# Performance work log

Hardware: AMD Instinct MI355X
Metric: run time of the kernel (lower is better)

## Reference

```python
import jax, jax.numpy as jnp
import numpy as np

UP_TIME = 1440.0
UP_DIST = 40.0
LOC_CNT = 100000
LOC_LEN = 131072
H = 256


def setup_inputs() -> dict:
    key = jax.random.key(0)
    ks = jax.random.split(key, 12)
    stdv = 1.0 / np.sqrt(H)
    u = lambda k, shape: jax.random.uniform(k, shape, jnp.float32, -stdv, stdv)
    return {
        "td_upper": jax.random.uniform(ks[0], (LOC_LEN,), jnp.float32),
        "td_lower": jax.random.uniform(ks[1], (LOC_LEN,), jnp.float32),
        "ld_upper": jax.random.uniform(ks[2], (LOC_LEN,), jnp.float32),
        "ld_lower": jax.random.uniform(ks[3], (LOC_LEN,), jnp.float32),
        "loc": jax.random.randint(ks[4], (LOC_LEN,), 0, LOC_CNT, jnp.int32),
        "hx": jax.random.normal(ks[5], (H, 1), jnp.float32),
        "weight_ih": u(ks[6], (H, H)),
        "weight_th_upper": u(ks[7], (H, H)),
        "weight_th_lower": u(ks[8], (H, H)),
        "weight_sh_upper": u(ks[9], (H, H)),
        "weight_sh_lower": u(ks[10], (H, H)),
        "location_weight": u(ks[11], (LOC_CNT, H)),
    }


def reference(td_upper, td_lower, ld_upper, ld_lower, loc, hx,
              weight_ih, weight_th_upper, weight_th_lower,
              weight_sh_upper, weight_sh_lower, location_weight):
    tu = jnp.clip(td_upper, 0.0, UP_TIME)
    tl = jnp.clip(td_lower, 0.0, UP_TIME)
    lu = jnp.clip(ld_upper, 0.0, UP_DIST)
    ll = jnp.clip(ld_lower, 0.0, UP_DIST)

    e = location_weight[loc]  # [L, H] gathered POI embeddings
    # Ttd[i] @ e[i] = (tu[i]*W_tu@e[i] + tl[i]*W_tl@e[i]) / (tu[i]+tl[i])
    a = jnp.einsum('hk,lk->lh', weight_th_upper, e)
    b = jnp.einsum('hk,lk->lh', weight_th_lower, e)
    t = (tu[:, None] * a + tl[:, None] * b) / (tu + tl)[:, None]  # [L, H]
    # Sld[i] @ t[i]
    c = jnp.einsum('hk,lk->lh', weight_sh_upper, t)
    d = jnp.einsum('hk,lk->lh', weight_sh_lower, t)
    s = (lu[:, None] * c + ll[:, None] * d) / (lu + ll)[:, None]  # [L, H]

    loc_vec = jnp.sum(s, axis=0)[:, None]  # [H, 1]
    usr_vec = weight_ih @ hx               # [H, 1]
    return jax.nn.sigmoid(loc_vec + usr_vec)
```

## Files before the change

kernel.cpp:

```cpp
#include <hip/hip_runtime.h>
#include <math.h>

#define H 256

__global__ __launch_bounds__(256) void strnn_scatter(
    const float* __restrict__ td_u, const float* __restrict__ td_l,
    const float* __restrict__ ld_u, const float* __restrict__ ld_l,
    const int* __restrict__ loc, float* __restrict__ W, int L, int Rpad)
{
    const int i = blockIdx.x * blockDim.x + threadIdx.x;
    if (i >= L) return;
    const float tu = fminf(fmaxf(td_u[i], 0.f), 1440.f);
    const float tl = fminf(fmaxf(td_l[i], 0.f), 1440.f);
    const float lu = fminf(fmaxf(ld_u[i], 0.f), 40.f);
    const float ll = fminf(fmaxf(ld_l[i], 0.f), 40.f);
    const float al = tu / (tu + tl);
    const float be = lu / (lu + ll);
    const int r = loc[i];
    atomicAdd(W + r,            be * al);
    atomicAdd(W + Rpad + r,     be * (1.f - al));
    atomicAdd(W + 2 * Rpad + r, (1.f - be) * al);
    atomicAdd(W + 3 * Rpad + r, (1.f - be) * (1.f - al));
}

__global__ __launch_bounds__(512) void strnn_accum(
    const float* __restrict__ W, const float* __restrict__ table,
    float* __restrict__ v, int R, int Rpad)
{
    __shared__ float s_red[8][4][H];
    const int t    = threadIdx.x;
    const int wave = t >> 6;
    const int lane = t & 63;
    const float* __restrict__ W0 = W;
    const float* __restrict__ W1 = W + Rpad;
    const float* __restrict__ W2 = W + 2 * (size_t)Rpad;
    const float* __restrict__ W3 = W + 3 * (size_t)Rpad;

    float4 a0 = {0,0,0,0}, a1 = {0,0,0,0}, a2 = {0,0,0,0}, a3 = {0,0,0,0};

    const int gw     = blockIdx.x * 8 + wave;
    const int stride = gridDim.x * 8 * 8;

    for (int r0 = gw * 8; r0 < R; r0 += stride) {
        float w0[8], w1[8], w2[8], w3[8];
        *(float4*)&w0[0] = *(const float4*)(W0 + r0);
        *(float4*)&w0[4] = *(const float4*)(W0 + r0 + 4);
        *(float4*)&w1[0] = *(const float4*)(W1 + r0);
        *(float4*)&w1[4] = *(const float4*)(W1 + r0 + 4);
        *(float4*)&w2[0] = *(const float4*)(W2 + r0);
        *(float4*)&w2[4] = *(const float4*)(W2 + r0 + 4);
        *(float4*)&w3[0] = *(const float4*)(W3 + r0);
        *(float4*)&w3[4] = *(const float4*)(W3 + r0 + 4);

        float4 e[8];
        #pragma unroll
        for (int u = 0; u < 8; ++u) {
            const int r = r0 + u;
            const bool live = (r < R) &&
                (w0[u] != 0.f || w1[u] != 0.f || w2[u] != 0.f || w3[u] != 0.f);
            const size_t roff = live ? (size_t)r * H : (size_t)0;
            e[u] = *(const float4*)(table + roff + 4 * lane);
        }
        #pragma unroll
        for (int u = 0; u < 8; ++u) {
            a0.x = fmaf(w0[u], e[u].x, a0.x);
            a0.y = fmaf(w0[u], e[u].y, a0.y);
            a0.z = fmaf(w0[u], e[u].z, a0.z);
            a0.w = fmaf(w0[u], e[u].w, a0.w);
            a1.x = fmaf(w1[u], e[u].x, a1.x);
            a1.y = fmaf(w1[u], e[u].y, a1.y);
            a1.z = fmaf(w1[u], e[u].z, a1.z);
            a1.w = fmaf(w1[u], e[u].w, a1.w);
            a2.x = fmaf(w2[u], e[u].x, a2.x);
            a2.y = fmaf(w2[u], e[u].y, a2.y);
            a2.z = fmaf(w2[u], e[u].z, a2.z);
            a2.w = fmaf(w2[u], e[u].w, a2.w);
            a3.x = fmaf(w3[u], e[u].x, a3.x);
            a3.y = fmaf(w3[u], e[u].y, a3.y);
            a3.z = fmaf(w3[u], e[u].z, a3.z);
            a3.w = fmaf(w3[u], e[u].w, a3.w);
        }
    }

    *(float4*)&s_red[wave][0][4 * lane] = a0;
    *(float4*)&s_red[wave][1][4 * lane] = a1;
    *(float4*)&s_red[wave][2][4 * lane] = a2;
    *(float4*)&s_red[wave][3][4 * lane] = a3;
    __syncthreads();
    const int col = t & 255;
    #pragma unroll
    for (int cc = 0; cc < 2; ++cc) {
        const int c = (t >> 8) * 2 + cc;
        float s = 0.f;
        #pragma unroll
        for (int w_ = 0; w_ < 8; ++w_)
            s += s_red[w_][c][col];
        atomicAdd(&v[c * H + col], s);
    }
}

__global__ __launch_bounds__(256) void strnn_mid(
    const float* __restrict__ Wtu, const float* __restrict__ Wtl,
    const float* __restrict__ Wih, const float* __restrict__ hx,
    const float* __restrict__ v, float* __restrict__ pqu)
{
    const int wave = (blockIdx.x * blockDim.x + threadIdx.x) >> 6;
    const int lane = threadIdx.x & 63;
    const float* v1 = v;
    const float* v2 = v + H;
    const float* v3 = v + 2 * H;
    const float* v4 = v + 3 * H;

    float p = 0.f, q = 0.f, u = 0.f;
    #pragma unroll
    for (int i = 0; i < H; i += 64) {
        const int k = i + lane;
        const float wtu = Wtu[wave * H + k];
        const float wtl = Wtl[wave * H + k];
        p = fmaf(wtu, v1[k], fmaf(wtl, v2[k], p));
        q = fmaf(wtu, v3[k], fmaf(wtl, v4[k], q));
        u = fmaf(Wih[wave * H + k], hx[k], u);
    }
    #pragma unroll
    for (int off = 32; off > 0; off >>= 1) {
        p += __shfl_down(p, off, 64);
        q += __shfl_down(q, off, 64);
        u += __shfl_down(u, off, 64);
    }
    if (lane == 0) {
        pqu[wave]         = p;
        pqu[H + wave]     = q;
        pqu[2 * H + wave] = u;
    }
}

__global__ __launch_bounds__(256) void strnn_out(
    const float* __restrict__ Wsu, const float* __restrict__ Wsl,
    const float* __restrict__ pqu, float* __restrict__ out)
{
    const int wave = (blockIdx.x * blockDim.x + threadIdx.x) >> 6;
    const int lane = threadIdx.x & 63;
    const float* p = pqu;
    const float* q = pqu + H;
    const float* u = pqu + 2 * H;

    float s = 0.f;
    #pragma unroll
    for (int i = 0; i < H; i += 64) {
        const int k = i + lane;
        s = fmaf(Wsu[wave * H + k], p[k], fmaf(Wsl[wave * H + k], q[k], s));
    }
    #pragma unroll
    for (int off = 32; off > 0; off >>= 1)
        s += __shfl_down(s, off, 64);
    if (lane == 0)
        out[wave] = 1.f / (1.f + expf(-(s + u[wave])));
}

extern "C" void kernel_launch(void* const* d_in, const int* in_sizes, int n_in,
                              void* d_out, int out_size, void* d_ws, size_t ws_size,
                              hipStream_t stream) {
    const float* td_u  = (const float*)d_in[0];
    const float* td_l  = (const float*)d_in[1];
    const float* ld_u  = (const float*)d_in[2];
    const float* ld_l  = (const float*)d_in[3];
    const int*   loc   = (const int*)d_in[4];
    const float* hx    = (const float*)d_in[5];
    const float* Wih   = (const float*)d_in[6];
    const float* Wtu   = (const float*)d_in[7];
    const float* Wtl   = (const float*)d_in[8];
    const float* Wsu   = (const float*)d_in[9];
    const float* Wsl   = (const float*)d_in[10];
    const float* table = (const float*)d_in[11];
    const int L = in_sizes[0];
    const int R = in_sizes[11] / H;
    const int Rpad = (R + 7) & ~7;

    float* W   = (float*)d_ws;
    float* v   = W + 4 * (size_t)Rpad;
    float* pqu = v + 4 * H;

    hipMemsetAsync(W, 0, (4 * (size_t)Rpad + 4 * H) * sizeof(float), stream);

    strnn_scatter<<<(L + 255) / 256, 256, 0, stream>>>(
        td_u, td_l, ld_u, ld_l, loc, W, L, Rpad);
    strnn_accum<<<256, 512, 0, stream>>>(W, table, v, R, Rpad);
    strnn_mid<<<64, 256, 0, stream>>>(Wtu, Wtl, Wih, hx, v, pqu);
    strnn_out<<<64, 256, 0, stream>>>(Wsu, Wsl, pqu, (float*)d_out);
}
```

Before: 203.5 us.

## Pack quantized fixed-point weights into two 64-bit atomics per element

Replaces the four float atomics per sequence element with two 64-bit integer atomics holding 24-bit fixed-point sums of alpha, beta, alpha*beta and a count. The four bilinear weights are rebuilt from those sums in the accumulation kernel. The change also drops the zero-row skip, so every table row is read, and doubles the accum grid with an occupancy hint. It cuts atomic traffic and makes the sums deterministic, but it adds quantization error and removes the branch that avoided loading unused rows.

After: 197.4 us. 3.0% less time.

```diff
diff --git a/kernel.cpp b/kernel.cpp
--- a/kernel.cpp
+++ b/kernel.cpp
@@ -2,11 +2,13 @@
 #include <math.h>
 
 #define H 256
+typedef unsigned long long u64;
 
 __global__ __launch_bounds__(256) void strnn_scatter(
     const float* __restrict__ td_u, const float* __restrict__ td_l,
     const float* __restrict__ ld_u, const float* __restrict__ ld_l,
-    const int* __restrict__ loc, float* __restrict__ W, int L, int Rpad)
+    const int* __restrict__ loc, u64* __restrict__ U1, u64* __restrict__ U2,
+    int L)
 {
     const int i = blockIdx.x * blockDim.x + threadIdx.x;
     if (i >= L) return;
@@ -16,25 +18,22 @@
     const float ll = fminf(fmaxf(ld_l[i], 0.f), 40.f);
     const float al = tu / (tu + tl);
     const float be = lu / (lu + ll);
+    const u64 alq = (u64)(unsigned)(al * 16777216.f + 0.5f);
+    const u64 beq = (u64)(unsigned)(be * 16777216.f + 0.5f);
+    const u64 abq = (u64)(unsigned)(al * be * 16777216.f + 0.5f);
     const int r = loc[i];
-    atomicAdd(W + r,            be * al);
-    atomicAdd(W + Rpad + r,     be * (1.f - al));
-    atomicAdd(W + 2 * Rpad + r, (1.f - be) * al);
-    atomicAdd(W + 3 * Rpad + r, (1.f - be) * (1.f - al));
+    atomicAdd(U1 + r, (alq << 32) | beq);
+    atomicAdd(U2 + r, (abq << 32) | 1ull);
 }
 
-__global__ __launch_bounds__(512) void strnn_accum(
-    const float* __restrict__ W, const float* __restrict__ table,
-    float* __restrict__ v, int R, int Rpad)
+__global__ __launch_bounds__(512, 4) void strnn_accum(
+    const u64* __restrict__ U1, const u64* __restrict__ U2,
+    const float* __restrict__ table, float* __restrict__ v, int R)
 {
     __shared__ float s_red[8][4][H];
     const int t    = threadIdx.x;
     const int wave = t >> 6;
     const int lane = t & 63;
-    const float* __restrict__ W0 = W;
-    const float* __restrict__ W1 = W + Rpad;
-    const float* __restrict__ W2 = W + 2 * (size_t)Rpad;
-    const float* __restrict__ W3 = W + 3 * (size_t)Rpad;
 
     float4 a0 = {0,0,0,0}, a1 = {0,0,0,0}, a2 = {0,0,0,0}, a3 = {0,0,0,0};
 
@@ -42,43 +41,48 @@
     const int stride = gridDim.x * 8 * 8;
 
     for (int r0 = gw * 8; r0 < R; r0 += stride) {
-        float w0[8], w1[8], w2[8], w3[8];
-        *(float4*)&w0[0] = *(const float4*)(W0 + r0);
-        *(float4*)&w0[4] = *(const float4*)(W0 + r0 + 4);
-        *(float4*)&w1[0] = *(const float4*)(W1 + r0);
-        *(float4*)&w1[4] = *(const float4*)(W1 + r0 + 4);
-        *(float4*)&w2[0] = *(const float4*)(W2 + r0);
-        *(float4*)&w2[4] = *(const float4*)(W2 + r0 + 4);
-        *(float4*)&w3[0] = *(const float4*)(W3 + r0);
-        *(float4*)&w3[4] = *(const float4*)(W3 + r0 + 4);
-
+        uint4 q1[4], q2[4];
+        #pragma unroll
+        for (int k = 0; k < 4; ++k) {
+            q1[k] = *(const uint4*)(U1 + r0 + 2 * k);
+            q2[k] = *(const uint4*)(U2 + r0 + 2 * k);
+        }
         float4 e[8];
         #pragma unroll
         for (int u = 0; u < 8; ++u) {
-            const int r = r0 + u;
-            const bool live = (r < R) &&
-                (w0[u] != 0.f || w1[u] != 0.f || w2[u] != 0.f || w3[u] != 0.f);
-            const size_t roff = live ? (size_t)r * H : (size_t)0;
-            e[u] = *(const float4*)(table + roff + 4 * lane);
+            int r = r0 + u;
+            r = (r < R) ? r : (R - 1);
+            e[u] = *(const float4*)(table + (size_t)r * H + 4 * lane);
         }
+        const float S = 5.9604644775390625e-8f;
         #pragma unroll
         for (int u = 0; u < 8; ++u) {
-            a0.x = fmaf(w0[u], e[u].x, a0.x);
-            a0.y = fmaf(w0[u], e[u].y, a0.y);
-            a0.z = fmaf(w0[u], e[u].z, a0.z);
-            a0.w = fmaf(w0[u], e[u].w, a0.w);
-            a1.x = fmaf(w1[u], e[u].x, a1.x);
-            a1.y = fmaf(w1[u], e[u].y, a1.y);
-            a1.z = fmaf(w1[u], e[u].z, a1.z);
-            a1.w = fmaf(w1[u], e[u].w, a1.w);
-            a2.x = fmaf(w2[u], e[u].x, a2.x);
-            a2.y = fmaf(w2[u], e[u].y, a2.y);
-            a2.z = fmaf(w2[u], e[u].z, a2.z);
-            a2.w = fmaf(w2[u], e[u].w, a2.w);
-            a3.x = fmaf(w3[u], e[u].x, a3.x);
-            a3.y = fmaf(w3[u], e[u].y, a3.y);
-            a3.z = fmaf(w3[u], e[u].z, a3.z);
-            a3.w = fmaf(w3[u], e[u].w, a3.w);
+            const uint4 q = q1[u >> 1];
+            const uint4 p = q2[u >> 1];
+            const float be_s = (float)((u & 1) ? q.z : q.x) * S;
+            const float al_s = (float)((u & 1) ? q.w : q.y) * S;
+            const float ab   = (float)((u & 1) ? p.w : p.y) * S;
+            const float n    = (float)((u & 1) ? p.z : p.x);
+            const float w0 = ab;
+            const float w1 = be_s - ab;
+            const float w2 = al_s - ab;
+            const float w3 = n - al_s - be_s + ab;
+            a0.x = fmaf(w0, e[u].x, a0.x);
+            a0.y = fmaf(w0, e[u].y, a0.y);
+            a0.z = fmaf(w0, e[u].z, a0.z);
+            a0.w = fmaf(w0, e[u].w, a0.w);
+            a1.x = fmaf(w1, e[u].x, a1.x);
+            a1.y = fmaf(w1, e[u].y, a1.y);
+            a1.z = fmaf(w1, e[u].z, a1.z);
+            a1.w = fmaf(w1, e[u].w, a1.w);
+            a2.x = fmaf(w2, e[u].x, a2.x);
+            a2.y = fmaf(w2, e[u].y, a2.y);
+            a2.z = fmaf(w2, e[u].z, a2.z);
+            a2.w = fmaf(w2, e[u].w, a2.w);
+            a3.x = fmaf(w3, e[u].x, a3.x);
+            a3.y = fmaf(w3, e[u].y, a3.y);
+            a3.z = fmaf(w3, e[u].z, a3.z);
+            a3.w = fmaf(w3, e[u].w, a3.w);
         }
     }
 
@@ -176,15 +180,17 @@
     const int R = in_sizes[11] / H;
     const int Rpad = (R + 7) & ~7;
 
-    float* W   = (float*)d_ws;
-    float* v   = W + 4 * (size_t)Rpad;
+    u64*   U1  = (u64*)d_ws;
+    u64*   U2  = U1 + Rpad;
+    float* v   = (float*)(U2 + Rpad);
     float* pqu = v + 4 * H;
 
-    hipMemsetAsync(W, 0, (4 * (size_t)Rpad + 4 * H) * sizeof(float), stream);
+    hipMemsetAsync(U1, 0, 2 * (size_t)Rpad * sizeof(u64) + 4 * H * sizeof(float),
+                   stream);
 
     strnn_scatter<<<(L + 255) / 256, 256, 0, stream>>>(
-        td_u, td_l, ld_u, ld_l, loc, W, L, Rpad);
-    strnn_accum<<<256, 512, 0, stream>>>(W, table, v, R, Rpad);
+        td_u, td_l, ld_u, ld_l, loc, U1, U2, L);
+    strnn_accum<<<512, 512, 0, stream>>>(U1, U2, table, v, R);
     strnn_mid<<<64, 256, 0, stream>>>(Wtu, Wtl, Wih, hx, v, pqu);
     strnn_out<<<64, 256, 0, stream>>>(Wsu, Wsl, pqu, (float*)d_out);
 }
```
